# Kernel optimization log

Measured on AMD Instinct MI355X. Metric: run time of the kernel, lower is better.

The kernel has to match this reference:

```python
import jax, jax.numpy as jnp
import numpy as np

B, N, DIN, DOUT, T, R, H = 4, 384, 128, 128, 4, 4, 8
DK = DOUT // H
SQRT_DK = float(np.sqrt(DK))


def setup_inputs() -> dict:
    key = jax.random.key(0)
    k = jax.random.split(key, 12)
    node_features = jax.random.normal(k[0], (B, N, DIN), jnp.float32)
    nt = jax.random.uniform(k[1], (B, N, T), dtype=jnp.float32)
    node_types_soft = nt / nt.sum(-1, keepdims=True)  # soft type distribution
    adj_matrix_soft = jax.random.uniform(k[2], (B, N, N), dtype=jnp.float32)
    et = jax.random.uniform(k[3], (B, N, N, R), dtype=jnp.float32)
    edge_types_soft = et / et.sum(-1, keepdims=True)  # soft relation distribution
    s = 0.05  # ~xavier scale for 128x128
    return dict(
        node_features=node_features,
        node_types_soft=node_types_soft,
        adj_matrix_soft=adj_matrix_soft,
        edge_types_soft=edge_types_soft,
        kw=jax.random.normal(k[4], (T, DIN, DOUT), jnp.float32) * s,
        kb=jnp.zeros((T, DOUT), jnp.float32),
        qw=jax.random.normal(k[5], (T, DIN, DOUT), jnp.float32) * s,
        qb=jnp.zeros((T, DOUT), jnp.float32),
        vw=jax.random.normal(k[6], (T, DIN, DOUT), jnp.float32) * s,
        vb=jnp.zeros((T, DOUT), jnp.float32),
        aw=jax.random.normal(k[7], (T, DOUT, DOUT), jnp.float32) * s,
        ab=jnp.zeros((T, DOUT), jnp.float32),
        norm_w=jnp.ones((T, DOUT), jnp.float32),
        norm_b=jnp.zeros((T, DOUT), jnp.float32),
        rel_pri=jnp.ones((R, H), jnp.float32),
        rel_att=jax.random.normal(k[8], (R, H, DK, DK), jnp.float32) * 0.1,
        rel_msg=jax.random.normal(k[9], (R, H, DK, DK), jnp.float32) * 0.1,
        skip=jnp.ones((T,), jnp.float32),
    )


def _forward(node_features, node_types_soft, adj_matrix_soft, edge_types_soft,
             kw, kb, qw, qb, vw, vb, aw, ab, norm_w, norm_b,
             rel_pri, rel_att, rel_msg, skip):
    Bq, Nn, _ = node_features.shape
    nt = node_types_soft
    # per-type Q/K/V projections: [B,N,T,H,DK]
    q = (jnp.einsum('bni,tid->bntd', node_features, qw) + qb).reshape(Bq, Nn, T, H, DK)
    kk = (jnp.einsum('bni,tid->bntd', node_features, kw) + kb).reshape(Bq, Nn, T, H, DK)
    v = (jnp.einsum('bni,tid->bntd', node_features, vw) + vb).reshape(Bq, Nn, T, H, DK)

    res_att = jnp.zeros((Bq, Nn, Nn, H), node_features.dtype)
    res_msg = jnp.zeros((Bq, Nn, Nn, H, DK), node_features.dtype)
    for r in range(R):  # small fixed relation count; types/heads fully vectorized
        kr = jnp.einsum('bjshe,hed->bjshd', kk, rel_att[r])
        vr = jnp.einsum('bjshe,hed->bjshd', v, rel_msg[r])
        # fold target-type mask (applied at node j in the original) into k: [B,N,Tt,Ts,H,DK]
        krt = kr[:, :, None] * nt[:, :, :, None, None, None]
        # P[b,i,j,s,h] = sum_{t,d} q[b,i,t,h,d] * nt[b,j,t] * kr[b,j,s,h,d], scaled
        P = jnp.einsum('bithd,bjtshd->bijsh', q, krt) * (rel_pri[r] / SQRT_DK)
        mask = edge_types_soft[..., r] * adj_matrix_soft  # [B,N,N]
        res_att = res_att + jnp.einsum('bijsh,bis->bijh', P, nt) * mask[..., None]
        res_msg = res_msg + jnp.einsum('bijsh,bis,bjshd->bijhd', P, nt, vr) * mask[..., None, None]

    att_sum = res_att.sum(axis=1, keepdims=True)
    safe = jnp.where(att_sum > 1e-6, att_sum, jnp.ones_like(att_sum))
    attw = (res_att / safe) * (att_sum > 1e-6).astype(res_att.dtype)
    agg = jnp.einsum('btsh,btshd->bthd', attw, res_msg).reshape(Bq, Nn, DOUT)

    trans = jnp.einsum('bnd,tdo->bnto', agg, aw) + ab
    trans = jax.nn.gelu(trans, approximate=False)  # dropout = identity at eval
    alpha = jax.nn.sigmoid(skip)[None, None, :, None]
    # in_dim == out_dim -> identity skip projection
    res = trans * alpha + node_features[:, :, None, :] * (1.0 - alpha)
    mean = res.mean(-1, keepdims=True)
    var = res.var(-1, keepdims=True)
    res = (res - mean) / jnp.sqrt(var + 1e-5) * norm_w + norm_b
    return (res * nt[..., None]).sum(axis=2)  # [B,N,DOUT]


def reference(node_features, node_types_soft, adj_matrix_soft, edge_types_soft,
              kw, kb, qw, qb, vw, vb, aw, ab, norm_w, norm_b,
              rel_pri, rel_att, rel_msg, skip):
    return _forward(node_features, node_types_soft, adj_matrix_soft, edge_types_soft,
                    kw, kb, qw, qb, vw, vb, aw, ab, norm_w, norm_b,
                    rel_pri, rel_att, rel_msg, skip)
```

## Files before the change

kernel.cpp:

```cpp
#include <hip/hip_runtime.h>
#include <math.h>

#define Bq 4
#define Nn 384
#define NB 1536
#define TT 4
#define RR 4
#define HH 8
#define DKk 16

typedef __attribute__((ext_vector_type(8))) short short8;
typedef __attribute__((ext_vector_type(4))) float f32x4;

__device__ __forceinline__ unsigned short f2bf(float f) {
  unsigned u = __float_as_uint(f);
  u += 0x7FFFu + ((u >> 16) & 1u);
  return (unsigned short)(u >> 16);
}

__device__ __forceinline__ void ld16(const float* __restrict__ p, float* o) {
  const float4* p4 = reinterpret_cast<const float4*>(p);
  float4 a = p4[0], b = p4[1], c = p4[2], d = p4[3];
  o[0]=a.x; o[1]=a.y; o[2]=a.z; o[3]=a.w;
  o[4]=b.x; o[5]=b.y; o[6]=b.z; o[7]=b.w;
  o[8]=c.x; o[9]=c.y; o[10]=c.z; o[11]=c.w;
  o[12]=d.x; o[13]=d.y; o[14]=d.z; o[15]=d.w;
}


__global__ __launch_bounds__(256) void k1a_qkv(
    const float* __restrict__ nf,
    const float* __restrict__ qw, const float* __restrict__ qb,
    const float* __restrict__ kw, const float* __restrict__ kb,
    const float* __restrict__ vw, const float* __restrict__ vb,
    float* __restrict__ q_ws, float* __restrict__ kv_k, float* __restrict__ kv_v)
{
  __shared__ float A_s[32][72];
  __shared__ float W_s[32][132];
  int mt = blockIdx.x, t = blockIdx.y, z = blockIdx.z;
  const float* W    = (z == 0) ? qw : ((z == 1) ? kw : vw);
  const float* bias = (z == 0) ? qb : ((z == 1) ? kb : vb);
  int tid = threadIdx.x;
  int colq = (tid & 31)*4, n8 = (tid >> 5)*8;
  float acc[8][4];
#pragma unroll
  for (int u = 0; u < 8; ++u)
#pragma unroll
    for (int c = 0; c < 4; ++c) acc[u][c] = 0.f;

  for (int kc = 0; kc < 4; ++kc) {
    __syncthreads();
    {
      int kk = tid & 31, nb0 = tid >> 5;
#pragma unroll
      for (int u = 0; u < 8; ++u)
        A_s[kk][nb0 + u*8] = nf[(size_t)(mt*64 + nb0 + u*8)*128 + kc*32 + kk];
#pragma unroll
      for (int u = 0; u < 4; ++u) {
        int idx = u*256 + tid;
        int wk = idx >> 5, c4 = (idx & 31)*4;
        *(float4*)&W_s[wk][c4] = *(const float4*)&W[(size_t)(t*128 + kc*32 + wk)*128 + c4];
      }
    }
    __syncthreads();
#pragma unroll
    for (int k = 0; k < 32; ++k) {
      float4 w4 = *(float4*)&W_s[k][colq];
      float a0[8];
      *(float4*)&a0[0] = *(float4*)&A_s[k][n8];
      *(float4*)&a0[4] = *(float4*)&A_s[k][n8 + 4];
#pragma unroll
      for (int u = 0; u < 8; ++u) {
        acc[u][0] += a0[u]*w4.x; acc[u][1] += a0[u]*w4.y;
        acc[u][2] += a0[u]*w4.z; acc[u][3] += a0[u]*w4.w;
      }
    }
  }
  float4 bv = *(const float4*)&bias[t*128 + colq];
#pragma unroll
  for (int u = 0; u < 8; ++u) {
    int node = mt*64 + n8 + u;
    float4 o;
    o.x = acc[u][0] + bv.x; o.y = acc[u][1] + bv.y;
    o.z = acc[u][2] + bv.z; o.w = acc[u][3] + bv.w;
    if (z == 0) {
      int h = colq >> 4, d = colq & 15;
      *(float4*)&q_ws[((size_t)h*NB + node)*64 + t*16 + d] = o;
    } else {
      float* dst = (z == 1) ? kv_k : kv_v;
      *(float4*)&dst[(size_t)node*512 + t*128 + colq] = o;
    }
  }
}

__global__ __launch_bounds__(256) void k1b_rel(
    const float* __restrict__ kv_k, const float* __restrict__ kv_v,
    const float* __restrict__ rel_att, const float* __restrict__ rel_msg,
    float* __restrict__ kr_ws, float* __restrict__ vr_ws)
{
  __shared__ float ra_s[4][16][16];
  __shared__ float rm_s[4][16][16];
  __shared__ float k_s[16][4][17];
  __shared__ float v_s[16][4][17];
  int nb = blockIdx.x, h = blockIdx.y;
  int n0 = nb*16;
  int tid = threadIdx.x;
#pragma unroll
  for (int u0 = 0; u0 < 4; ++u0) {
    int u = u0*256 + tid;
    int r = u >> 8, e = (u >> 4) & 15, d = u & 15;
    ra_s[r][e][d] = rel_att[((size_t)(r*8 + h)*16 + e)*16 + d];
    rm_s[r][e][d] = rel_msg[((size_t)(r*8 + h)*16 + e)*16 + d];
    int nl = u >> 6, s = (u >> 4) & 3, e2 = u & 15;
    k_s[nl][s][e2] = kv_k[(size_t)(n0 + nl)*512 + s*128 + h*16 + e2];
    v_s[nl][s][e2] = kv_v[(size_t)(n0 + nl)*512 + s*128 + h*16 + e2];
  }
  __syncthreads();
  int nl = tid >> 4, dq = tid & 15;
  size_t obase = ((size_t)h*NB + n0 + nl)*256;
#pragma unroll
  for (int r = 0; r < 4; ++r)
#pragma unroll
    for (int s = 0; s < 4; ++s) {
      float aK = 0.f, aV = 0.f;
#pragma unroll
      for (int e = 0; e < 16; ++e) {
        aK += k_s[nl][s][e] * ra_s[r][e][dq];
        aV += v_s[nl][s][e] * rm_s[r][e][dq];
      }
      kr_ws[obase + r*64 + s*16 + dq] = aK;
      vr_ws[obase + r*64 + s*16 + dq] = aV;
    }
}

__global__ __launch_bounds__(256,2) void k2_att(
    const float* __restrict__ nt, const float* __restrict__ adj,
    const float* __restrict__ ets, const float* __restrict__ rel_pri,
    const float* __restrict__ q_ws, const float* __restrict__ kr_ws,
    float* __restrict__ res_att, float* __restrict__ att_part)
{
  __shared__ float q_s[16*68];
  __shared__ float kr_s[32*260];
  __shared__ float ntj_s[32*4];
  __shared__ float nti_s[16*4];
  int it = blockIdx.x, h = blockIdx.y, b = blockIdx.z;
  int i0 = it*16;
  int tid = threadIdx.x;
  int j_l = tid>>3, ig = (tid>>1)&3, dh = tid&1;
  {
    int i = tid>>4, f = (tid&15)*4;
    float4 qv = *(const float4*)&q_ws[((size_t)(h*NB) + b*Nn + i0 + i)*64 + f];
    *(float4*)&q_s[i*68 + f] = qv;
  }
  if (tid < 64) nti_s[tid] = nt[(size_t)(b*Nn + i0 + (tid>>2))*TT + (tid&3)];
  float crr[4];
#pragma unroll
  for (int r = 0; r < 4; ++r) crr[r] = rel_pri[r*HH+h]*0.25f;

  for (int jc = 0; jc < 12; ++jc) {
    __syncthreads();
    {
      int js = tid>>3, gb = tid&7;
      const float* src = &kr_ws[((size_t)(h*NB) + b*Nn + jc*32 + js)*256];
      float* dst = &kr_s[js*260];
#pragma unroll
      for (int gl = 0; gl < 8; ++gl) {
        int g = gl*8 + gb;
        float4 v = *(const float4*)&src[g*4];
        int r = g>>4, s = (g>>2)&3, qd = g&3;
        int gd = (qd>>1)*32 + r*8 + s*2 + (qd&1);
        *(float4*)&dst[gd*4] = v;
      }
      if (tid < 128) ntj_s[tid] = nt[(size_t)(b*Nn + jc*32 + (tid>>2))*TT + (tid&3)];
    }
    __syncthreads();
    int j = jc*32 + j_l;
    float nt0 = ntj_s[j_l*4+0], nt1 = ntj_s[j_l*4+1];
    float nt2 = ntj_s[j_l*4+2], nt3 = ntj_s[j_l*4+3];
    float qn[4][8];
#pragma unroll
    for (int il = 0; il < 4; ++il) {
      int ib = (ig*4 + il)*68 + dh*8;
#pragma unroll
      for (int dp = 0; dp < 8; ++dp)
        qn[il][dp] = q_s[ib+dp]*nt0 + q_s[ib+16+dp]*nt1 + q_s[ib+32+dp]*nt2 + q_s[ib+48+dp]*nt3;
    }
    float mar[4][4];
#pragma unroll
    for (int il = 0; il < 4; ++il) {
      int i = i0 + ig*4 + il;
      float a = adj[((size_t)b*Nn + i)*Nn + j];
      float4 e4 = *(const float4*)&ets[(((size_t)b*Nn + i)*Nn + j)*RR];
      mar[il][0]=e4.x*a; mar[il][1]=e4.y*a; mar[il][2]=e4.z*a; mar[il][3]=e4.w*a;
    }
    float acc[4] = {0.f,0.f,0.f,0.f};
    const float* kbp = &kr_s[j_l*260 + dh*128];
#pragma unroll
    for (int r = 0; r < 4; ++r) {
      float mr0 = mar[0][r]*crr[r], mr1 = mar[1][r]*crr[r];
      float mr2 = mar[2][r]*crr[r], mr3 = mar[3][r]*crr[r];
#pragma unroll
      for (int s = 0; s < 4; ++s) {
        float kk[8];
        *(float4*)&kk[0] = *(const float4*)&kbp[r*32 + s*8];
        *(float4*)&kk[4] = *(const float4*)&kbp[r*32 + s*8 + 4];
        float d0=0,d1=0,d2=0,d3=0;
#pragma unroll
        for (int dp = 0; dp < 8; ++dp) {
          d0 += qn[0][dp]*kk[dp]; d1 += qn[1][dp]*kk[dp];
          d2 += qn[2][dp]*kk[dp]; d3 += qn[3][dp]*kk[dp];
        }
        d0 += __shfl_xor(d0,1); d1 += __shfl_xor(d1,1);
        d2 += __shfl_xor(d2,1); d3 += __shfl_xor(d3,1);
        acc[0] += mr0*nti_s[(ig*4+0)*4+s]*d0;
        acc[1] += mr1*nti_s[(ig*4+1)*4+s]*d1;
        acc[2] += mr2*nti_s[(ig*4+2)*4+s]*d2;
        acc[3] += mr3*nti_s[(ig*4+3)*4+s]*d3;
      }
    }
    if (dh == 0) {
#pragma unroll
      for (int il = 0; il < 4; ++il)
        res_att[((size_t)(b*HH + h)*Nn + i0 + ig*4 + il)*Nn + j] = acc[il];
    }
    float v = acc[0] + acc[1] + acc[2] + acc[3];
    v += __shfl_xor(v, 2);
    v += __shfl_xor(v, 4);
    if ((tid & 7) == 0)
      att_part[(size_t)it*12288 + (size_t)(b*HH + h)*Nn + j] = v;
  }
}

__global__ __launch_bounds__(256) void kb_inv(
    const float* __restrict__ att_part, float* __restrict__ att_inv)
{
  int idx = blockIdx.x*256 + threadIdx.x;
  float s = 0.f;
#pragma unroll
  for (int p = 0; p < 24; ++p) s += att_part[(size_t)p*12288 + idx];
  att_inv[idx] = (s > 1e-6f) ? 1.f/s : 0.f;
}

__global__ __launch_bounds__(256) void kc_agg(
    const float* __restrict__ nt, const float* __restrict__ adj,
    const float* __restrict__ ets, const float* __restrict__ rel_pri,
    const float* __restrict__ q_ws, const float* __restrict__ kr_ws,
    const float* __restrict__ vr_ws, const float* __restrict__ res_att,
    const float* __restrict__ att_inv, float* __restrict__ agg)
{
  __shared__ __align__(16) unsigned short B_lds[4][64*72];
  __shared__ __align__(16) unsigned short vr_lds[64*72];
  __shared__ __align__(16) unsigned short Z_lds[4][16*72];
  __shared__ float ntj_s[64*4];
  int it = blockIdx.x, jp = blockIdx.y, bh = blockIdx.z;
  int b = bh >> 3, h = bh & 7;
  int tid = threadIdx.x, w = tid >> 6, l = tid & 63;
  int ib = it*64 + w*16;
  int irow = ib + (l & 15);
  int iz = ib + ((l >> 4) << 2);
  int lq = (l >> 4) * 8;
  short8 af[4][2];
  {
    float q0[8], q1[8];
    const float* qp = &q_ws[((size_t)h*NB + b*Nn + irow)*64];
    *(float4*)&q0[0] = *(const float4*)&qp[lq];
    *(float4*)&q0[4] = *(const float4*)&qp[lq + 4];
    *(float4*)&q1[0] = *(const float4*)&qp[32 + lq];
    *(float4*)&q1[4] = *(const float4*)&qp[32 + lq + 4];
    float4 ntiv = *(const float4*)&nt[(size_t)(b*Nn + irow)*4];
    float nta[4] = {ntiv.x, ntiv.y, ntiv.z, ntiv.w};
#pragma unroll
    for (int s = 0; s < 4; ++s)
#pragma unroll
      for (int e = 0; e < 8; ++e) {
        af[s][0][e] = (short)f2bf(q0[e]*nta[s]);
        af[s][1][e] = (short)f2bf(q1[e]*nta[s]);
      }
  }
  float crv[4];
#pragma unroll
  for (int r = 0; r < 4; ++r) crv[r] = rel_pri[r*HH + h]*0.25f;
  f32x4 agg_acc = {0.f,0.f,0.f,0.f};

  for (int jc = 0; jc < 3; ++jc) {
    int j0 = jp*192 + jc*64;
    __syncthreads();
    ntj_s[tid] = nt[(size_t)(b*Nn + j0 + (tid>>2))*4 + (tid&3)];
    float attwv[4][4], adjc[4][4];
#pragma unroll
    for (int tj = 0; tj < 4; ++tj) {
      int j = j0 + tj*16 + (l & 15);
      float inv = att_inv[(size_t)bh*Nn + j];
#pragma unroll
      for (int p = 0; p < 4; ++p) {
        int i = iz + p;
        attwv[tj][p] = res_att[((size_t)bh*Nn + i)*Nn + j] * inv;
        adjc[tj][p] = adj[((size_t)b*Nn + i)*Nn + j];
      }
    }
    for (int r = 0; r < 4; ++r) {
      __syncthreads();
      {
        float kv[16];
        ld16(&kr_ws[((size_t)h*NB + b*Nn + j0 + l)*256 + r*64 + w*16], kv);
        const float* nrow = &ntj_s[l*4];
#pragma unroll
        for (int t = 0; t < 4; ++t) {
          float sc = nrow[t];
#pragma unroll
          for (int dq = 0; dq < 2; ++dq) {
            short8 v;
#pragma unroll
            for (int e = 0; e < 8; ++e) v[e] = (short)f2bf(kv[dq*8 + e]*sc);
            *(short8*)&B_lds[w][l*72 + t*16 + dq*8] = v;
          }
        }
        float vv[16];
        ld16(&vr_ws[((size_t)h*NB + b*Nn + j0 + l)*256 + r*64 + w*16], vv);
#pragma unroll
        for (int d = 0; d < 16; ++d)
          vr_lds[(w*16 + d)*72 + l] = f2bf(vv[d]);
      }
      __syncthreads();
      float coef[4][4];
#pragma unroll
      for (int tj = 0; tj < 4; ++tj)
#pragma unroll
        for (int p = 0; p < 4; ++p) {
          int i = iz + p, j = j0 + tj*16 + (l & 15);
          coef[tj][p] = ets[(((size_t)b*Nn + i)*Nn + j)*4 + r] * adjc[tj][p] * crv[r] * attwv[tj][p];
        }
#pragma unroll
      for (int s = 0; s < 4; ++s) {
        f32x4 wacc[4];
#pragma unroll
        for (int tj = 0; tj < 4; ++tj) wacc[tj] = (f32x4){0.f,0.f,0.f,0.f};
#pragma unroll
        for (int tj = 0; tj < 4; ++tj) {
          short8 b0 = *(const short8*)&B_lds[s][(tj*16 + (l & 15))*72 + lq];
          short8 b1 = *(const short8*)&B_lds[s][(tj*16 + (l & 15))*72 + 32 + lq];
          wacc[tj] = __builtin_amdgcn_mfma_f32_16x16x32_bf16(af[s][0], b0, wacc[tj], 0, 0, 0);
          wacc[tj] = __builtin_amdgcn_mfma_f32_16x16x32_bf16(af[s][1], b1, wacc[tj], 0, 0, 0);
        }
#pragma unroll
        for (int tj = 0; tj < 4; ++tj)
#pragma unroll
          for (int p = 0; p < 4; ++p)
            Z_lds[w][(((l >> 4)*4) + p)*72 + tj*16 + (l & 15)] = f2bf(wacc[tj][p]*coef[tj][p]);
#pragma unroll
        for (int kj = 0; kj < 2; ++kj) {
          short8 zf = *(const short8*)&Z_lds[w][(l & 15)*72 + kj*32 + lq];
          short8 vf = *(const short8*)&vr_lds[(s*16 + (l & 15))*72 + kj*32 + lq];
          agg_acc = __builtin_amdgcn_mfma_f32_16x16x32_bf16(zf, vf, agg_acc, 0, 0, 0);
        }
      }
    }
  }
#pragma unroll
  for (int p = 0; p < 4; ++p)
    atomicAdd(&agg[((size_t)b*Nn + iz + p)*128 + h*16 + (l & 15)], agg_acc[p]);
}

__global__ __launch_bounds__(128) void k5_out(
    const float* __restrict__ agg_ws, const float* __restrict__ nf,
    const float* __restrict__ nt, const float* __restrict__ aw,
    const float* __restrict__ ab, const float* __restrict__ norm_w,
    const float* __restrict__ norm_b, const float* __restrict__ skip,
    float* __restrict__ out)
{
  __shared__ float agg_s[128];
  __shared__ float red[4];
  int n = blockIdx.x, b = blockIdx.y;
  int o = threadIdx.x;
  size_t node = (size_t)b*Nn + n;
  agg_s[o] = agg_ws[node*128 + o];
  __syncthreads();
  float nfo = nf[node*128 + o];
  float outacc = 0.f;
  for (int t = 0; t < TT; ++t) {
    float a = ab[t*128 + o];
    for (int dd = 0; dd < 128; ++dd) a += agg_s[dd] * aw[(size_t)(t*128 + dd)*128 + o];
    float g = 0.5f * a * (1.f + erff(a * 0.70710678118654752f));
    float alpha = 1.f / (1.f + expf(-skip[t]));
    float res = g*alpha + nfo*(1.f - alpha);
    float s1 = res, s2 = res*res;
#pragma unroll
    for (int m = 32; m >= 1; m >>= 1) { s1 += __shfl_xor(s1, m); s2 += __shfl_xor(s2, m); }
    int w = o >> 6;
    if ((o & 63) == 0) { red[w*2] = s1; red[w*2 + 1] = s2; }
    __syncthreads();
    float tot1 = red[0] + red[2], tot2 = red[1] + red[3];
    __syncthreads();
    float mean = tot1 * (1.f/128.f);
    float var  = tot2 * (1.f/128.f) - mean*mean;
    float nrm = (res - mean) * rsqrtf(var + 1e-5f) * norm_w[t*128 + o] + norm_b[t*128 + o];
    outacc += nrm * nt[node*TT + t];
  }
  out[node*128 + o] = outacc;
}

extern "C" void kernel_launch(void* const* d_in, const int* in_sizes, int n_in,
                              void* d_out, int out_size, void* d_ws, size_t ws_size,
                              hipStream_t stream) {
  const float* nf      = (const float*)d_in[0];
  const float* nts     = (const float*)d_in[1];
  const float* adj     = (const float*)d_in[2];
  const float* ets     = (const float*)d_in[3];
  const float* kw      = (const float*)d_in[4];
  const float* kb      = (const float*)d_in[5];
  const float* qw      = (const float*)d_in[6];
  const float* qb      = (const float*)d_in[7];
  const float* vw      = (const float*)d_in[8];
  const float* vb      = (const float*)d_in[9];
  const float* aw      = (const float*)d_in[10];
  const float* ab      = (const float*)d_in[11];
  const float* normw   = (const float*)d_in[12];
  const float* normb   = (const float*)d_in[13];
  const float* rel_pri = (const float*)d_in[14];
  const float* rel_att = (const float*)d_in[15];
  const float* rel_msg = (const float*)d_in[16];
  const float* skip    = (const float*)d_in[17];
  (void)in_sizes; (void)n_in; (void)out_size; (void)ws_size;

  float* ws = (float*)d_ws;
  float* q_ws    = ws;
  float* kr_ws   = q_ws + 786432;
  float* vr_ws   = kr_ws + 3145728;
  float* res_att = vr_ws + 3145728;
  float* att_part= res_att + 4718592;
  float* att_inv = att_part + 294912;
  float* agg_ws  = att_inv + 12288;
  float* kv_k = res_att;
  float* kv_v = res_att + 786432;

  hipMemsetAsync(agg_ws, 0, (size_t)196608*4, stream);
  hipLaunchKernelGGL(k1a_qkv, dim3(24, 4, 3), dim3(256), 0, stream,
                     nf, qw, qb, kw, kb, vw, vb, q_ws, kv_k, kv_v);
  hipLaunchKernelGGL(k1b_rel, dim3(96, 8), dim3(256), 0, stream,
                     kv_k, kv_v, rel_att, rel_msg, kr_ws, vr_ws);
  hipLaunchKernelGGL(k2_att, dim3(24, 8, 4), dim3(256), 0, stream,
                     nts, adj, ets, rel_pri, q_ws, kr_ws, res_att, att_part);
  hipLaunchKernelGGL(kb_inv, dim3(48), dim3(256), 0, stream, att_part, att_inv);
  hipLaunchKernelGGL(kc_agg, dim3(6, 2, 32), dim3(256), 0, stream,
                     nts, adj, ets, rel_pri, q_ws, kr_ws, vr_ws, res_att, att_inv, agg_ws);
  hipLaunchKernelGGL(k5_out, dim3(384, 4), dim3(128), 0, stream,
                     agg_ws, nf, nts, aw, ab, normw, normb, skip, (float*)d_out);
}
```

Measured before the change: 228.2 us.

## Split kc_agg over j-chunks and prefetch next relation's K/V into registers

The aggregation kernel now gives each block a single 64-column j chunk instead of looping over three, tripling the grid (6x6x32) for more parallelism at the cost of more atomicAdds into agg. Inside, the loads for the next relation's kr/vr rows are issued before the MFMA work of the current relation, and the per-edge coefficient (res_att*inv*adj) is precomputed once with rel_pri folded into the B-operand scaling. Full __syncthreads are replaced by an LDS-only waitcnt plus s_barrier so global loads in flight do not stall the barrier. The q fragment setup is repeated per block, which adds redundant work.

```diff
diff --git a/kernel.cpp b/kernel.cpp
--- a/kernel.cpp
+++ b/kernel.cpp
@@ -25,6 +25,11 @@
   o[4]=b.x; o[5]=b.y; o[6]=b.z; o[7]=b.w;
   o[8]=c.x; o[9]=c.y; o[10]=c.z; o[11]=c.w;
   o[12]=d.x; o[13]=d.y; o[14]=d.z; o[15]=d.w;
+}
+
+__device__ __forceinline__ void bar_lds() {
+  asm volatile("s_waitcnt lgkmcnt(0)" ::: "memory");
+  __builtin_amdgcn_s_barrier();
 }
 
 
@@ -251,14 +256,16 @@
   __shared__ __align__(16) unsigned short B_lds[4][64*72];
   __shared__ __align__(16) unsigned short vr_lds[64*72];
   __shared__ __align__(16) unsigned short Z_lds[4][16*72];
-  __shared__ float ntj_s[64*4];
-  int it = blockIdx.x, jp = blockIdx.y, bh = blockIdx.z;
+  __shared__ float ntj_s[256];
+  int it = blockIdx.x, jc = blockIdx.y, bh = blockIdx.z;
   int b = bh >> 3, h = bh & 7;
   int tid = threadIdx.x, w = tid >> 6, l = tid & 63;
+  int j0 = jc*64;
   int ib = it*64 + w*16;
   int irow = ib + (l & 15);
   int iz = ib + ((l >> 4) << 2);
   int lq = (l >> 4) * 8;
+  ntj_s[tid] = nt[(size_t)(b*Nn + j0 + (tid>>2))*4 + (tid&3)];
   short8 af[4][2];
   {
     float q0[8], q1[8];
@@ -280,80 +287,90 @@
   float crv[4];
 #pragma unroll
   for (int r = 0; r < 4; ++r) crv[r] = rel_pri[r*HH + h]*0.25f;
+  float cw[4][4];
+  int eo[4][4];
+  const float* ebase = ets + (size_t)b*Nn*Nn*4;
+#pragma unroll
+  for (int tj = 0; tj < 4; ++tj) {
+    int j = j0 + tj*16 + (l & 15);
+    float inv = att_inv[(size_t)bh*Nn + j];
+#pragma unroll
+    for (int p = 0; p < 4; ++p) {
+      int i = iz + p;
+      cw[tj][p] = res_att[((size_t)bh*Nn + i)*Nn + j] * inv
+                * adj[((size_t)b*Nn + i)*Nn + j];
+      eo[tj][p] = (i*Nn + j)*4;
+    }
+  }
   f32x4 agg_acc = {0.f,0.f,0.f,0.f};
-
-  for (int jc = 0; jc < 3; ++jc) {
-    int j0 = jp*192 + jc*64;
-    __syncthreads();
-    ntj_s[tid] = nt[(size_t)(b*Nn + j0 + (tid>>2))*4 + (tid&3)];
-    float attwv[4][4], adjc[4][4];
-#pragma unroll
-    for (int tj = 0; tj < 4; ++tj) {
-      int j = j0 + tj*16 + (l & 15);
-      float inv = att_inv[(size_t)bh*Nn + j];
-#pragma unroll
-      for (int p = 0; p < 4; ++p) {
-        int i = iz + p;
-        attwv[tj][p] = res_att[((size_t)bh*Nn + i)*Nn + j] * inv;
-        adjc[tj][p] = adj[((size_t)b*Nn + i)*Nn + j];
-      }
-    }
-    for (int r = 0; r < 4; ++r) {
-      __syncthreads();
-      {
-        float kv[16];
-        ld16(&kr_ws[((size_t)h*NB + b*Nn + j0 + l)*256 + r*64 + w*16], kv);
-        const float* nrow = &ntj_s[l*4];
-#pragma unroll
-        for (int t = 0; t < 4; ++t) {
-          float sc = nrow[t];
-#pragma unroll
-          for (int dq = 0; dq < 2; ++dq) {
-            short8 v;
-#pragma unroll
-            for (int e = 0; e < 8; ++e) v[e] = (short)f2bf(kv[dq*8 + e]*sc);
-            *(short8*)&B_lds[w][l*72 + t*16 + dq*8] = v;
-          }
+  int js = tid >> 2, ss = tid & 3;
+  const float* krp = &kr_ws[((size_t)h*NB + b*Nn + j0 + js)*256 + ss*16];
+  const float* vrp = &vr_ws[((size_t)h*NB + b*Nn + j0 + js)*256 + ss*16];
+  float kvA[16], vvA[16];
+  ld16(krp, kvA);
+  ld16(vrp, vvA);
+  bar_lds();
+
+#pragma unroll
+  for (int r = 0; r < 4; ++r) {
+    if (r) bar_lds();
+    {
+      float crr = crv[r];
+      float4 ntjv = *(const float4*)&ntj_s[js*4];
+      float nta[4] = {ntjv.x*crr, ntjv.y*crr, ntjv.z*crr, ntjv.w*crr};
+#pragma unroll
+      for (int t = 0; t < 4; ++t) {
+#pragma unroll
+        for (int dq = 0; dq < 2; ++dq) {
+          short8 v;
+#pragma unroll
+          for (int e = 0; e < 8; ++e) v[e] = (short)f2bf(kvA[dq*8 + e]*nta[t]);
+          *(short8*)&B_lds[ss][js*72 + t*16 + dq*8] = v;
         }
-        float vv[16];
-        ld16(&vr_ws[((size_t)h*NB + b*Nn + j0 + l)*256 + r*64 + w*16], vv);
-#pragma unroll
-        for (int d = 0; d < 16; ++d)
-          vr_lds[(w*16 + d)*72 + l] = f2bf(vv[d]);
-      }
-      __syncthreads();
-      float coef[4][4];
+      }
+#pragma unroll
+      for (int d = 0; d < 16; ++d)
+        vr_lds[(ss*16 + d)*72 + js] = f2bf(vvA[d]);
+    }
+    float kvB[16], vvB[16];
+    if (r < 3) {
+      ld16(krp + (r+1)*64, kvB);
+      ld16(vrp + (r+1)*64, vvB);
+    }
+    bar_lds();
+    float coef[4][4];
+#pragma unroll
+    for (int tj = 0; tj < 4; ++tj)
+#pragma unroll
+      for (int p = 0; p < 4; ++p)
+        coef[tj][p] = ebase[eo[tj][p] + r] * cw[tj][p];
+#pragma unroll
+    for (int s = 0; s < 4; ++s) {
+      f32x4 wacc[4];
+#pragma unroll
+      for (int tj = 0; tj < 4; ++tj) wacc[tj] = (f32x4){0.f,0.f,0.f,0.f};
+#pragma unroll
+      for (int tj = 0; tj < 4; ++tj) {
+        short8 b0 = *(const short8*)&B_lds[s][(tj*16 + (l & 15))*72 + lq];
+        short8 b1 = *(const short8*)&B_lds[s][(tj*16 + (l & 15))*72 + 32 + lq];
+        wacc[tj] = __builtin_amdgcn_mfma_f32_16x16x32_bf16(af[s][0], b0, wacc[tj], 0, 0, 0);
+        wacc[tj] = __builtin_amdgcn_mfma_f32_16x16x32_bf16(af[s][1], b1, wacc[tj], 0, 0, 0);
+      }
 #pragma unroll
       for (int tj = 0; tj < 4; ++tj)
 #pragma unroll
-        for (int p = 0; p < 4; ++p) {
-          int i = iz + p, j = j0 + tj*16 + (l & 15);
-          coef[tj][p] = ets[(((size_t)b*Nn + i)*Nn + j)*4 + r] * adjc[tj][p] * crv[r] * attwv[tj][p];
-        }
-#pragma unroll
-      for (int s = 0; s < 4; ++s) {
-        f32x4 wacc[4];
-#pragma unroll
-        for (int tj = 0; tj < 4; ++tj) wacc[tj] = (f32x4){0.f,0.f,0.f,0.f};
-#pragma unroll
-        for (int tj = 0; tj < 4; ++tj) {
-          short8 b0 = *(const short8*)&B_lds[s][(tj*16 + (l & 15))*72 + lq];
-          short8 b1 = *(const short8*)&B_lds[s][(tj*16 + (l & 15))*72 + 32 + lq];
-          wacc[tj] = __builtin_amdgcn_mfma_f32_16x16x32_bf16(af[s][0], b0, wacc[tj], 0, 0, 0);
-          wacc[tj] = __builtin_amdgcn_mfma_f32_16x16x32_bf16(af[s][1], b1, wacc[tj], 0, 0, 0);
-        }
-#pragma unroll
-        for (int tj = 0; tj < 4; ++tj)
-#pragma unroll
-          for (int p = 0; p < 4; ++p)
-            Z_lds[w][(((l >> 4)*4) + p)*72 + tj*16 + (l & 15)] = f2bf(wacc[tj][p]*coef[tj][p]);
-#pragma unroll
-        for (int kj = 0; kj < 2; ++kj) {
-          short8 zf = *(const short8*)&Z_lds[w][(l & 15)*72 + kj*32 + lq];
-          short8 vf = *(const short8*)&vr_lds[(s*16 + (l & 15))*72 + kj*32 + lq];
-          agg_acc = __builtin_amdgcn_mfma_f32_16x16x32_bf16(zf, vf, agg_acc, 0, 0, 0);
-        }
-      }
+        for (int p = 0; p < 4; ++p)
+          Z_lds[w][(((l >> 4)*4) + p)*72 + tj*16 + (l & 15)] = f2bf(wacc[tj][p]*coef[tj][p]);
+#pragma unroll
+      for (int kj = 0; kj < 2; ++kj) {
+        short8 zf = *(const short8*)&Z_lds[w][(l & 15)*72 + kj*32 + lq];
+        short8 vf = *(const short8*)&vr_lds[(s*16 + (l & 15))*72 + kj*32 + lq];
+        agg_acc = __builtin_amdgcn_mfma_f32_16x16x32_bf16(zf, vf, agg_acc, 0, 0, 0);
+      }
+    }
+    if (r < 3) {
+#pragma unroll
+      for (int e = 0; e < 16; ++e) { kvA[e] = kvB[e]; vvA[e] = vvB[e]; }
     }
   }
 #pragma unroll
@@ -441,7 +458,7 @@
   hipLaunchKernelGGL(k2_att, dim3(24, 8, 4), dim3(256), 0, stream,
                      nts, adj, ets, rel_pri, q_ws, kr_ws, res_att, att_part);
   hipLaunchKernelGGL(kb_inv, dim3(48), dim3(256), 0, stream, att_part, att_inv);
-  hipLaunchKernelGGL(kc_agg, dim3(6, 2, 32), dim3(256), 0, stream,
+  hipLaunchKernelGGL(kc_agg, dim3(6, 6, 32), dim3(256), 0, stream,
                      nts, adj, ets, rel_pri, q_ws, kr_ws, vr_ws, res_att, att_inv, agg_ws);
   hipLaunchKernelGGL(k5_out, dim3(384, 4), dim3(128), 0, stream,
                      agg_ws, nf, nts, aw, ab, normw, normb, skip, (float*)d_out);
```

After: 204.3 us. 10.5% less time.
